# Kernel optimization log

Hardware: AMD Instinct MI355X
Metric: run time of the kernel (lower is better)

## Reference

```python
import jax, jax.numpy as jnp
import numpy as np

B, T, C = 2, 4096, 1024
H = 16            # n_head (== n_groups == n_kv_heads)
HD = C // H       # head_dim = 64
W = 256           # window_size
ROPE_BASE = 10000.0


def _rope(x):
    # x: (B, H, T, HD); rotate interleaved pairs with position along axis 2
    t = x.shape[2]
    inv_freq = 1.0 / (ROPE_BASE ** (jnp.arange(0, HD, 2, dtype=jnp.float32) / HD))  # (HD/2,)
    freqs = jnp.arange(t, dtype=jnp.float32)[:, None] * inv_freq[None, :]           # (T, HD/2)
    cos = jnp.cos(freqs)[None, None].astype(x.dtype)
    sin = jnp.sin(freqs)[None, None].astype(x.dtype)
    x1, x2 = x[..., 0::2], x[..., 1::2]
    o1 = x1 * cos - x2 * sin
    o2 = x1 * sin + x2 * cos
    return jnp.stack([o1, o2], axis=-1).reshape(x.shape)


def setup_inputs() -> dict:
    key = jax.random.key(0)
    ks = jax.random.split(key, 5)
    s = 1.0 / np.sqrt(C)
    return {
        "x": jax.random.normal(ks[0], (B, T, C), dtype=jnp.float32),
        "wq": jax.random.normal(ks[1], (C, C), dtype=jnp.float32) * s,
        "wk": jax.random.normal(ks[2], (C, C), dtype=jnp.float32) * s,
        "wv": jax.random.normal(ks[3], (C, C), dtype=jnp.float32) * s,
        "wo": jax.random.normal(ks[4], (C, C), dtype=jnp.float32) * s,
    }


def reference(x, wq, wk, wv, wo):
    # projections (Linear stores (out, in) -> x @ w.T)
    q = jnp.einsum('btc,oc->bto', x, wq).reshape(B, T, H, HD).transpose(0, 2, 1, 3)
    k = jnp.einsum('btc,oc->bto', x, wk).reshape(B, T, H, HD).transpose(0, 2, 1, 3)
    v = jnp.einsum('btc,oc->bto', x, wv).reshape(B, T, H, HD).transpose(0, 2, 1, 3)

    q = _rope(q)
    k = _rope(k)

    nW = T // W
    qw = q.reshape(B, H, nW, W, HD)
    kw = k.reshape(B, H, nW, W, HD)
    vw = v.reshape(B, H, nW, W, HD)

    scale = 1.0 / jnp.sqrt(jnp.asarray(HD, dtype=q.dtype))
    att = jnp.einsum('bhnqd,bhnkd->bhnqk', qw, kw) * scale   # per-window, no causal mask
    att = jax.nn.softmax(att, axis=-1)
    yw = jnp.einsum('bhnqk,bhnkd->bhnqd', att, vw)

    y = yw.reshape(B, H, T, HD).transpose(0, 2, 1, 3).reshape(B, T, C)
    return jnp.einsum('btc,oc->bto', y, wo)
```

## Files before the change

### kernel.cpp

```cpp
#include <hip/hip_runtime.h>
#include <math.h>

typedef float f32x4 __attribute__((ext_vector_type(4)));
typedef __bf16 bf16x8 __attribute__((ext_vector_type(8)));
typedef unsigned short ushort_t;

#define MFMA16(a, b, c) __builtin_amdgcn_mfma_f32_16x16x32_bf16((a), (b), (c), 0, 0, 0)

static __device__ __forceinline__ ushort_t f2bf(float f) {
  union { float f; unsigned u; } v; v.f = f;
  unsigned u = v.u;
  return (ushort_t)((u + 0x7FFFu + ((u >> 16) & 1u)) >> 16);
}
static __device__ __forceinline__ float bf2f(ushort_t h) {
  union { unsigned u; float f; } v; v.u = ((unsigned)h) << 16;
  return v.f;
}
static __device__ __forceinline__ void gl_lds16(const void* g, void* lds_uniform) {
  __builtin_amdgcn_global_load_lds(
      (const __attribute__((address_space(1))) unsigned int*)g,
      (__attribute__((address_space(3))) unsigned int*)lds_uniform, 16, 0, 0);
}

__global__ void prep(const float* __restrict__ x,
                     const float* __restrict__ wq, const float* __restrict__ wk,
                     const float* __restrict__ wv, const float* __restrict__ wo,
                     ushort_t* __restrict__ Xb, ushort_t* __restrict__ Wqb,
                     ushort_t* __restrict__ Wkb, ushort_t* __restrict__ Wvb,
                     ushort_t* __restrict__ Wob, float2* __restrict__ cs) {
  const int bid = blockIdx.x;
  if (bid < 12288) {
    const float* src;
    ushort_t* dst;
    int i;
    if (bid < 8192) {
      src = x; dst = Xb;
      i = bid * 256 + threadIdx.x;
    } else {
      const int wi = (bid - 8192) >> 10;
      src = (wi == 0) ? wq : (wi == 1) ? wk : (wi == 2) ? wv : wo;
      dst = (wi == 0) ? Wqb : (wi == 1) ? Wkb : (wi == 2) ? Wvb : Wob;
      i = ((bid - 8192) & 1023) * 256 + threadIdx.x;
    }
    f32x4 v = ((const f32x4*)src)[i];
    ushort4 o;
    o.x = f2bf(v.x); o.y = f2bf(v.y); o.z = f2bf(v.z); o.w = f2bf(v.w);
    ((ushort4*)dst)[i] = o;
  } else {
    int idx = (bid - 12288) * 256 + threadIdx.x;
    int pos = idx >> 5, i = idx & 31;
    double inv = exp2(-(double)i * 0.41524101186092029);
    double th = (double)pos * inv;
    double s, c;
    sincos(th, &s, &c);
    cs[idx] = make_float2((float)c, (float)s);
  }
}

template <int OUTBF>
__global__ __launch_bounds__(512, 2) void gemm8(
    const ushort_t* __restrict__ A,
    const ushort_t* __restrict__ W0, const ushort_t* __restrict__ W1, const ushort_t* __restrict__ W2,
    void* __restrict__ C0, void* __restrict__ C1, void* __restrict__ C2,
    int K, int N) {
  __shared__ __align__(16) char smem[98304];
  const int z = blockIdx.z;
  const ushort_t* W = (z == 0) ? W0 : (z == 1 ? W1 : W2);
  void* Cv = (z == 0) ? C0 : (z == 1 ? C1 : C2);

  const int t = threadIdx.x;
  const int lane = t & 63;
  const int l15 = lane & 15, quad = lane >> 4;
  const int wave = t >> 6;
  const int wm = wave >> 1, wn = wave & 1;
  const int bm = blockIdx.x, bn = blockIdx.y;

  const int r0 = t >> 3;
  const int gc = (t & 7) ^ (r0 & 7);
  const ushort_t* Ag = A + (size_t)(bm * 256 + r0) * K + gc * 8;
  const ushort_t* Wg = W + (size_t)(bn * 128 + r0) * K + gc * 8;
  const size_t p64K = (size_t)64 * K;
  char* ldsw = smem + wave * 1024;

  const int sl0 = (quad ^ (l15 & 7)) * 16;
  const int aoff = (wm * 64 + l15) * 128 + sl0;
  const int boff = 65536 + (wn * 64 + l15) * 128 + sl0;

  const int KT = K >> 6;

  const f32x4 zero4 = {0.f, 0.f, 0.f, 0.f};
  f32x4 acc[4][4];
#pragma unroll
  for (int i = 0; i < 4; ++i)
#pragma unroll
    for (int j = 0; j < 4; ++j) acc[i][j] = zero4;

  auto stA = [&](int buf, int p, int k0) {
    gl_lds16(Ag + p64K * p + k0, ldsw + buf * 32768 + p * 8192);
  };
  auto stB = [&](int buf, int p, int k0) {
    gl_lds16(Wg + p64K * p + k0, ldsw + 65536 + buf * 16384 + p * 8192);
  };

  stA(0, 0, 0); stA(0, 1, 0); stA(0, 2, 0); stA(0, 3, 0);
  stB(0, 0, 0); stB(0, 1, 0);
  stA(1, 0, 64); stA(1, 1, 64); stA(1, 2, 64); stA(1, 3, 64);
  asm volatile("s_waitcnt vmcnt(4)" ::: "memory");
  __builtin_amdgcn_s_barrier();

  bf16x8 af[4][2], bfr[4][2];

  for (int j = 0; j < KT; ++j) {
    const int cb = j & 1, nb = cb ^ 1;
    const char* Ab = smem + cb * 32768;
    const char* Bb = smem + cb * 16384;

#pragma unroll
    for (int m = 0; m < 4; ++m) {
      const int o = aoff + m * 2048;
      af[m][0] = *(const bf16x8*)(Ab + o);
      af[m][1] = *(const bf16x8*)(Ab + (o ^ 64));
    }
#pragma unroll
    for (int n = 0; n < 2; ++n) {
      const int o = boff + n * 2048;
      bfr[n][0] = *(const bf16x8*)(Bb + o);
      bfr[n][1] = *(const bf16x8*)(Bb + (o ^ 64));
    }
    if (j + 1 < KT) {
      stB(nb, 0, (j + 1) * 64);
      stB(nb, 1, (j + 1) * 64);
    }
    __builtin_amdgcn_s_barrier();
    asm volatile("s_waitcnt lgkmcnt(0)" ::: "memory");
    __builtin_amdgcn_sched_barrier(0);
    __builtin_amdgcn_s_setprio(1);
#pragma unroll
    for (int m = 0; m < 4; ++m)
#pragma unroll
      for (int n = 0; n < 2; ++n) {
        acc[m][n] = MFMA16(af[m][0], bfr[n][0], acc[m][n]);
        acc[m][n] = MFMA16(af[m][1], bfr[n][1], acc[m][n]);
      }
    __builtin_amdgcn_s_setprio(0);
    __builtin_amdgcn_sched_barrier(0);
    __builtin_amdgcn_s_barrier();

#pragma unroll
    for (int n = 2; n < 4; ++n) {
      const int o = boff + n * 2048;
      bfr[n][0] = *(const bf16x8*)(Bb + o);
      bfr[n][1] = *(const bf16x8*)(Bb + (o ^ 64));
    }
    if (j + 2 < KT) {
      stA(cb, 0, (j + 2) * 64);
      stA(cb, 1, (j + 2) * 64);
      stA(cb, 2, (j + 2) * 64);
      stA(cb, 3, (j + 2) * 64);
      asm volatile("s_waitcnt vmcnt(4)" ::: "memory");
    } else if (j + 1 < KT) {
      asm volatile("s_waitcnt vmcnt(0)" ::: "memory");
    }
    __builtin_amdgcn_s_barrier();
    asm volatile("s_waitcnt lgkmcnt(0)" ::: "memory");
    __builtin_amdgcn_sched_barrier(0);
    __builtin_amdgcn_s_setprio(1);
#pragma unroll
    for (int m = 0; m < 4; ++m)
#pragma unroll
      for (int n = 2; n < 4; ++n) {
        acc[m][n] = MFMA16(af[m][0], bfr[n][0], acc[m][n]);
        acc[m][n] = MFMA16(af[m][1], bfr[n][1], acc[m][n]);
      }
    __builtin_amdgcn_s_setprio(0);
    __builtin_amdgcn_sched_barrier(0);
    __builtin_amdgcn_s_barrier();
  }

  const int rbase = bm * 256 + wm * 64 + quad * 4;
  const int cbase = bn * 128 + wn * 64 + l15;
#pragma unroll
  for (int m = 0; m < 4; ++m)
#pragma unroll
    for (int n = 0; n < 4; ++n)
#pragma unroll
      for (int r = 0; r < 4; ++r) {
        size_t idx = (size_t)(rbase + m * 16 + r) * N + (cbase + n * 16);
        if (OUTBF)
          ((ushort_t*)Cv)[idx] = f2bf(acc[m][n][r]);
        else
          ((float*)Cv)[idx] = acc[m][n][r];
      }
}

static __device__ __forceinline__ void rope8(const ushort_t* __restrict__ g,
                                             ushort_t* __restrict__ lds,
                                             const float2* __restrict__ cs4, float scale) {
  uint4 raw = *(const uint4*)g;
  unsigned rw[4] = {raw.x, raw.y, raw.z, raw.w};
  ushort_t o[8];
#pragma unroll
  for (int m = 0; m < 4; ++m) {
    float x1 = bf2f((ushort_t)(rw[m] & 0xffffu));
    float x2 = bf2f((ushort_t)(rw[m] >> 16));
    float2 sc = cs4[m];
    o[2 * m]     = f2bf((x1 * sc.x - x2 * sc.y) * scale);
    o[2 * m + 1] = f2bf((x1 * sc.y + x2 * sc.x) * scale);
  }
  uint4 w;
  w.x = (unsigned)o[0] | ((unsigned)o[1] << 16);
  w.y = (unsigned)o[2] | ((unsigned)o[3] << 16);
  w.z = (unsigned)o[4] | ((unsigned)o[5] << 16);
  w.w = (unsigned)o[6] | ((unsigned)o[7] << 16);
  *(uint4*)lds = w;
}

__global__ __launch_bounds__(256, 2) void attn(
    const ushort_t* __restrict__ Qb, const ushort_t* __restrict__ Kb,
    const ushort_t* __restrict__ Vb, ushort_t* __restrict__ Yb,
    const float2* __restrict__ cs) {
  __shared__ __align__(16) ushort_t smem[27648];
  ushort_t* Qs = smem;
  ushort_t* Ks = smem + 9216;
  ushort_t* Vt = smem;
  ushort_t* Pc = smem + 16896;

  const int t = threadIdx.x;
  const int lane = t & 63, wave = t >> 6;
  const int l15 = lane & 15, quad = lane >> 4;
  const int win = blockIdx.x >> 1, slice = blockIdx.x & 1;
  const int h = blockIdx.y, b = blockIdx.z;
  const int kBase = win * 256, qBase = kBase + slice * 128;
  const size_t gbase = ((size_t)b * 4096) * 1024 + h * 64;

  const int sr = t >> 3;
  const int c0 = (t & 7) * 8;

#pragma unroll
  for (int p = 0; p < 4; ++p) {
    int r = p * 32 + sr;
    rope8(Qb + gbase + (size_t)(qBase + r) * 1024 + c0, Qs + r * 72 + c0,
          cs + (qBase + r) * 32 + (c0 >> 1), 0.125f);
  }
#pragma unroll
  for (int p = 0; p < 8; ++p) {
    int r = p * 32 + sr;
    rope8(Kb + gbase + (size_t)(kBase + r) * 1024 + c0, Ks + r * 72 + c0,
          cs + (kBase + r) * 32 + (c0 >> 1), 1.0f);
  }
  __syncthreads();

  const int qw = wave * 32;
  const f32x4 zero4 = {0.f, 0.f, 0.f, 0.f};
  f32x4 S[2][16];
#pragma unroll
  for (int i = 0; i < 2; ++i)
#pragma unroll
    for (int j = 0; j < 16; ++j) S[i][j] = zero4;
#pragma unroll
  for (int ks = 0; ks < 2; ++ks) {
    bf16x8 a0 = *(const bf16x8*)&Qs[(qw + l15) * 72 + ks * 32 + quad * 8];
    bf16x8 a1 = *(const bf16x8*)&Qs[(qw + 16 + l15) * 72 + ks * 32 + quad * 8];
#pragma unroll
    for (int j = 0; j < 16; ++j) {
      bf16x8 bk = *(const bf16x8*)&Ks[(j * 16 + l15) * 72 + ks * 32 + quad * 8];
      S[0][j] = MFMA16(a0, bk, S[0][j]);
      S[1][j] = MFMA16(a1, bk, S[1][j]);
    }
  }

  float linv[2][4];
#pragma unroll
  for (int i = 0; i < 2; ++i)
#pragma unroll
    for (int r = 0; r < 4; ++r) {
      float mx = S[i][0][r];
#pragma unroll
      for (int j = 1; j < 16; ++j) mx = fmaxf(mx, S[i][j][r]);
      mx = fmaxf(mx, __shfl_xor(mx, 1));
      mx = fmaxf(mx, __shfl_xor(mx, 2));
      mx = fmaxf(mx, __shfl_xor(mx, 4));
      mx = fmaxf(mx, __shfl_xor(mx, 8));
      float sum = 0.f;
#pragma unroll
      for (int j = 0; j < 16; ++j) {
        float e = __expf(S[i][j][r] - mx);
        S[i][j][r] = e;
        sum += e;
      }
      sum += __shfl_xor(sum, 1);
      sum += __shfl_xor(sum, 2);
      sum += __shfl_xor(sum, 4);
      sum += __shfl_xor(sum, 8);
      linv[i][r] = 1.0f / sum;
    }
  __syncthreads();

#pragma unroll
  for (int p = 0; p < 8; ++p) {
    int k = p * 32 + sr;
    uint4 raw = *(const uint4*)(Vb + gbase + (size_t)(kBase + k) * 1024 + c0);
    ushort_t vv[8];
    vv[0] = raw.x & 0xffffu; vv[1] = raw.x >> 16;
    vv[2] = raw.y & 0xffffu; vv[3] = raw.y >> 16;
    vv[4] = raw.z & 0xffffu; vv[5] = raw.z >> 16;
    vv[6] = raw.w & 0xffffu; vv[7] = raw.w >> 16;
#pragma unroll
    for (int e = 0; e < 8; ++e) {
      int ee = (e + (t & 7)) & 7;
      Vt[(c0 + ee) * 264 + k] = vv[ee];
    }
  }

  auto writeP = [&](int kc) {
#pragma unroll
    for (int i = 0; i < 2; ++i)
#pragma unroll
      for (int jj = 0; jj < 4; ++jj) {
        int j = kc * 4 + jj;
#pragma unroll
        for (int r = 0; r < 4; ++r)
          Pc[(qw + i * 16 + quad * 4 + r) * 72 + jj * 16 + l15] = f2bf(S[i][j][r]);
      }
  };

  writeP(0);
  __syncthreads();

  f32x4 O[2][4];
#pragma unroll
  for (int i = 0; i < 2; ++i)
#pragma unroll
    for (int jd = 0; jd < 4; ++jd) O[i][jd] = zero4;

  for (int kc = 0; kc < 4; ++kc) {
#pragma unroll
    for (int ks = 0; ks < 2; ++ks) {
      bf16x8 a0 = *(const bf16x8*)&Pc[(qw + l15) * 72 + ks * 32 + quad * 8];
      bf16x8 a1 = *(const bf16x8*)&Pc[(qw + 16 + l15) * 72 + ks * 32 + quad * 8];
#pragma unroll
      for (int jd = 0; jd < 4; ++jd) {
        bf16x8 bv = *(const bf16x8*)&Vt[(jd * 16 + l15) * 264 + kc * 64 + ks * 32 + quad * 8];
        O[0][jd] = MFMA16(a0, bv, O[0][jd]);
        O[1][jd] = MFMA16(a1, bv, O[1][jd]);
      }
    }
    if (kc < 3) {
      __syncthreads();
      writeP(kc + 1);
      __syncthreads();
    }
  }

#pragma unroll
  for (int i = 0; i < 2; ++i)
#pragma unroll
    for (int jd = 0; jd < 4; ++jd)
#pragma unroll
      for (int r = 0; r < 4; ++r) {
        int row = qBase + qw + i * 16 + quad * 4 + r;
        int col = jd * 16 + l15;
        Yb[gbase + (size_t)row * 1024 + col] = f2bf(O[i][jd][r] * linv[i][r]);
      }
}

extern "C" void kernel_launch(void* const* d_in, const int* in_sizes, int n_in,
                              void* d_out, int out_size, void* d_ws, size_t ws_size,
                              hipStream_t stream) {
  (void)in_sizes; (void)n_in; (void)out_size; (void)ws_size;
  const float* x  = (const float*)d_in[0];
  const float* wq = (const float*)d_in[1];
  const float* wk = (const float*)d_in[2];
  const float* wv = (const float*)d_in[3];
  const float* wo = (const float*)d_in[4];

  char* ws = (char*)d_ws;
  ushort_t* Xb  = (ushort_t*)(ws);
  ushort_t* Wqb = (ushort_t*)(ws + 16777216);
  ushort_t* Wkb = Wqb + 1048576;
  ushort_t* Wvb = Wkb + 1048576;
  ushort_t* Wob = Wvb + 1048576;
  ushort_t* Qb  = (ushort_t*)(ws + 25165824);
  ushort_t* Kb  = Qb + 8388608;
  ushort_t* Vb  = Kb + 8388608;
  ushort_t* Yb  = Vb + 8388608;
  float2*   cs  = (float2*)(ws + 92274688);

  prep<<<dim3(12800), dim3(256), 0, stream>>>(x, wq, wk, wv, wo,
                                              Xb, Wqb, Wkb, Wvb, Wob, cs);

  gemm8<1><<<dim3(32, 8, 3), dim3(512), 0, stream>>>(
      Xb, Wqb, Wkb, Wvb, (void*)Qb, (void*)Kb, (void*)Vb, 1024, 1024);

  attn<<<dim3(32, 16, 2), dim3(256), 0, stream>>>(Qb, Kb, Vb, Yb, cs);

  gemm8<0><<<dim3(32, 8, 1), dim3(512), 0, stream>>>(
      Yb, Wob, Wob, Wob, d_out, d_out, d_out, 1024, 1024);
}
```

Before: 208.0 us.

## Enlarge GEMM block tile to 256x256 with four-phase pipelined K loop

The GEMM block tile grows from 256x128 to 256x256. Each wave now computes 128x64 outputs with an 8x4 accumulator array, and the grid halves along N. The K loop is split into four MFMA phases that interleave LDS fragment reads with staggered global-to-LDS prefetches of A and B, using a double-buffered 128KB shared memory. This raises arithmetic intensity and cuts global/LDS traffic per FLOP, at the cost of more registers, more LDS (likely one block per CU), and fewer blocks (384 and 128 instead of 768 and 256).

```diff
diff --git a/kernel.cpp b/kernel.cpp
--- a/kernel.cpp
+++ b/kernel.cpp
@@ -63,7 +63,7 @@
     const ushort_t* __restrict__ W0, const ushort_t* __restrict__ W1, const ushort_t* __restrict__ W2,
     void* __restrict__ C0, void* __restrict__ C1, void* __restrict__ C2,
     int K, int N) {
-  __shared__ __align__(16) char smem[98304];
+  __shared__ __align__(16) char smem[131072];
   const int z = blockIdx.z;
   const ushort_t* W = (z == 0) ? W0 : (z == 1 ? W1 : W2);
   void* Cv = (z == 0) ? C0 : (z == 1 ? C1 : C2);
@@ -72,64 +72,66 @@
   const int lane = t & 63;
   const int l15 = lane & 15, quad = lane >> 4;
   const int wave = t >> 6;
-  const int wm = wave >> 1, wn = wave & 1;
+  const int wm = wave >> 2, wn = wave & 3;
   const int bm = blockIdx.x, bn = blockIdx.y;
 
   const int r0 = t >> 3;
   const int gc = (t & 7) ^ (r0 & 7);
-  const ushort_t* Ag = A + (size_t)(bm * 256 + r0) * K + gc * 8;
-  const ushort_t* Wg = W + (size_t)(bn * 128 + r0) * K + gc * 8;
-  const size_t p64K = (size_t)64 * K;
+  const ushort_t* AgB = A + (size_t)(bm * 256 + r0) * K + gc * 8;
+  const ushort_t* WgB = W + (size_t)(bn * 256 + r0) * K + gc * 8;
+  const size_t q64K = (size_t)64 * K;
   char* ldsw = smem + wave * 1024;
 
   const int sl0 = (quad ^ (l15 & 7)) * 16;
-  const int aoff = (wm * 64 + l15) * 128 + sl0;
-  const int boff = 65536 + (wn * 64 + l15) * 128 + sl0;
+  const int aoff = (wm * 128 + l15) * 128 + sl0;
+  const int boff = 32768 + (wn * 64 + l15) * 128 + sl0;
 
   const int KT = K >> 6;
 
   const f32x4 zero4 = {0.f, 0.f, 0.f, 0.f};
-  f32x4 acc[4][4];
-#pragma unroll
-  for (int i = 0; i < 4; ++i)
+  f32x4 acc[8][4];
+#pragma unroll
+  for (int i = 0; i < 8; ++i)
 #pragma unroll
     for (int j = 0; j < 4; ++j) acc[i][j] = zero4;
 
-  auto stA = [&](int buf, int p, int k0) {
-    gl_lds16(Ag + p64K * p + k0, ldsw + buf * 32768 + p * 8192);
+  auto stA = [&](int buf, int q, int kt) {
+    gl_lds16(AgB + (size_t)q * q64K + (size_t)kt * 64, ldsw + buf * 65536 + q * 8192);
   };
-  auto stB = [&](int buf, int p, int k0) {
-    gl_lds16(Wg + p64K * p + k0, ldsw + 65536 + buf * 16384 + p * 8192);
+  auto stB = [&](int buf, int q, int kt) {
+    gl_lds16(WgB + (size_t)q * q64K + (size_t)kt * 64, ldsw + buf * 65536 + 32768 + q * 8192);
   };
 
-  stA(0, 0, 0); stA(0, 1, 0); stA(0, 2, 0); stA(0, 3, 0);
-  stB(0, 0, 0); stB(0, 1, 0);
-  stA(1, 0, 64); stA(1, 1, 64); stA(1, 2, 64); stA(1, 3, 64);
-  asm volatile("s_waitcnt vmcnt(4)" ::: "memory");
+#pragma unroll
+  for (int q = 0; q < 4; ++q) stA(0, q, 0);
+#pragma unroll
+  for (int q = 0; q < 4; ++q) stB(0, q, 0);
+#pragma unroll
+  for (int q = 0; q < 4; ++q) stA(1, q, 1);
+#pragma unroll
+  for (int q = 0; q < 4; ++q) stB(1, q, 1);
+  asm volatile("s_waitcnt vmcnt(8)" ::: "memory");
   __builtin_amdgcn_s_barrier();
 
-  bf16x8 af[4][2], bfr[4][2];
+  bf16x8 af[4][2], b01[2][2], b23[2][2];
 
   for (int j = 0; j < KT; ++j) {
-    const int cb = j & 1, nb = cb ^ 1;
-    const char* Ab = smem + cb * 32768;
-    const char* Bb = smem + cb * 16384;
+    const int cb = j & 1;
+    const char* bufb = smem + cb * 65536;
+    const bool pf = (j + 2 < KT);
+    const int k2 = j + 2;
 
 #pragma unroll
     for (int m = 0; m < 4; ++m) {
       const int o = aoff + m * 2048;
-      af[m][0] = *(const bf16x8*)(Ab + o);
-      af[m][1] = *(const bf16x8*)(Ab + (o ^ 64));
+      af[m][0] = *(const bf16x8*)(bufb + o);
+      af[m][1] = *(const bf16x8*)(bufb + (o ^ 64));
     }
 #pragma unroll
     for (int n = 0; n < 2; ++n) {
       const int o = boff + n * 2048;
-      bfr[n][0] = *(const bf16x8*)(Bb + o);
-      bfr[n][1] = *(const bf16x8*)(Bb + (o ^ 64));
-    }
-    if (j + 1 < KT) {
-      stB(nb, 0, (j + 1) * 64);
-      stB(nb, 1, (j + 1) * 64);
+      b01[n][0] = *(const bf16x8*)(bufb + o);
+      b01[n][1] = *(const bf16x8*)(bufb + (o ^ 64));
     }
     __builtin_amdgcn_s_barrier();
     asm volatile("s_waitcnt lgkmcnt(0)" ::: "memory");
@@ -139,48 +141,82 @@
     for (int m = 0; m < 4; ++m)
 #pragma unroll
       for (int n = 0; n < 2; ++n) {
-        acc[m][n] = MFMA16(af[m][0], bfr[n][0], acc[m][n]);
-        acc[m][n] = MFMA16(af[m][1], bfr[n][1], acc[m][n]);
+        acc[m][n] = MFMA16(af[m][0], b01[n][0], acc[m][n]);
+        acc[m][n] = MFMA16(af[m][1], b01[n][1], acc[m][n]);
       }
     __builtin_amdgcn_s_setprio(0);
     __builtin_amdgcn_sched_barrier(0);
     __builtin_amdgcn_s_barrier();
 
 #pragma unroll
-    for (int n = 2; n < 4; ++n) {
-      const int o = boff + n * 2048;
-      bfr[n][0] = *(const bf16x8*)(Bb + o);
-      bfr[n][1] = *(const bf16x8*)(Bb + (o ^ 64));
-    }
-    if (j + 2 < KT) {
-      stA(cb, 0, (j + 2) * 64);
-      stA(cb, 1, (j + 2) * 64);
-      stA(cb, 2, (j + 2) * 64);
-      stA(cb, 3, (j + 2) * 64);
-      asm volatile("s_waitcnt vmcnt(4)" ::: "memory");
+    for (int n = 0; n < 2; ++n) {
+      const int o = boff + (n + 2) * 2048;
+      b23[n][0] = *(const bf16x8*)(bufb + o);
+      b23[n][1] = *(const bf16x8*)(bufb + (o ^ 64));
+    }
+    if (pf) { stA(cb, 0, k2); stA(cb, 2, k2); }
+    __builtin_amdgcn_s_barrier();
+    asm volatile("s_waitcnt lgkmcnt(0)" ::: "memory");
+    __builtin_amdgcn_sched_barrier(0);
+    __builtin_amdgcn_s_setprio(1);
+#pragma unroll
+    for (int m = 0; m < 4; ++m)
+#pragma unroll
+      for (int n = 0; n < 2; ++n) {
+        acc[m][n + 2] = MFMA16(af[m][0], b23[n][0], acc[m][n + 2]);
+        acc[m][n + 2] = MFMA16(af[m][1], b23[n][1], acc[m][n + 2]);
+      }
+    __builtin_amdgcn_s_setprio(0);
+    __builtin_amdgcn_sched_barrier(0);
+    __builtin_amdgcn_s_barrier();
+
+#pragma unroll
+    for (int m = 0; m < 4; ++m) {
+      const int o = aoff + (m + 4) * 2048;
+      af[m][0] = *(const bf16x8*)(bufb + o);
+      af[m][1] = *(const bf16x8*)(bufb + (o ^ 64));
+    }
+    if (pf) { stB(cb, 0, k2); stB(cb, 1, k2); }
+    __builtin_amdgcn_s_barrier();
+    asm volatile("s_waitcnt lgkmcnt(0)" ::: "memory");
+    __builtin_amdgcn_sched_barrier(0);
+    __builtin_amdgcn_s_setprio(1);
+#pragma unroll
+    for (int m = 0; m < 4; ++m)
+#pragma unroll
+      for (int n = 0; n < 2; ++n) {
+        acc[m + 4][n] = MFMA16(af[m][0], b01[n][0], acc[m + 4][n]);
+        acc[m + 4][n] = MFMA16(af[m][1], b01[n][1], acc[m + 4][n]);
+      }
+    __builtin_amdgcn_s_setprio(0);
+    __builtin_amdgcn_sched_barrier(0);
+    __builtin_amdgcn_s_barrier();
+
+    if (pf) {
+      stA(cb, 1, k2); stA(cb, 3, k2);
+      stB(cb, 2, k2); stB(cb, 3, k2);
+      asm volatile("s_waitcnt vmcnt(8)" ::: "memory");
     } else if (j + 1 < KT) {
       asm volatile("s_waitcnt vmcnt(0)" ::: "memory");
     }
     __builtin_amdgcn_s_barrier();
-    asm volatile("s_waitcnt lgkmcnt(0)" ::: "memory");
-    __builtin_amdgcn_sched_barrier(0);
     __builtin_amdgcn_s_setprio(1);
 #pragma unroll
     for (int m = 0; m < 4; ++m)
 #pragma unroll
-      for (int n = 2; n < 4; ++n) {
-        acc[m][n] = MFMA16(af[m][0], bfr[n][0], acc[m][n]);
-        acc[m][n] = MFMA16(af[m][1], bfr[n][1], acc[m][n]);
+      for (int n = 0; n < 2; ++n) {
+        acc[m + 4][n + 2] = MFMA16(af[m][0], b23[n][0], acc[m + 4][n + 2]);
+        acc[m + 4][n + 2] = MFMA16(af[m][1], b23[n][1], acc[m + 4][n + 2]);
       }
     __builtin_amdgcn_s_setprio(0);
     __builtin_amdgcn_sched_barrier(0);
     __builtin_amdgcn_s_barrier();
   }
 
-  const int rbase = bm * 256 + wm * 64 + quad * 4;
-  const int cbase = bn * 128 + wn * 64 + l15;
-#pragma unroll
-  for (int m = 0; m < 4; ++m)
+  const int rbase = bm * 256 + wm * 128 + quad * 4;
+  const int cbase = bn * 256 + wn * 64 + l15;
+#pragma unroll
+  for (int m = 0; m < 8; ++m)
 #pragma unroll
     for (int n = 0; n < 4; ++n)
 #pragma unroll
@@ -389,11 +425,11 @@
   prep<<<dim3(12800), dim3(256), 0, stream>>>(x, wq, wk, wv, wo,
                                               Xb, Wqb, Wkb, Wvb, Wob, cs);
 
-  gemm8<1><<<dim3(32, 8, 3), dim3(512), 0, stream>>>(
+  gemm8<1><<<dim3(32, 4, 3), dim3(512), 0, stream>>>(
       Xb, Wqb, Wkb, Wvb, (void*)Qb, (void*)Kb, (void*)Vb, 1024, 1024);
 
   attn<<<dim3(32, 16, 2), dim3(256), 0, stream>>>(Qb, Kb, Vb, Yb, cs);
 
-  gemm8<0><<<dim3(32, 8, 1), dim3(512), 0, stream>>>(
+  gemm8<0><<<dim3(32, 4, 1), dim3(512), 0, stream>>>(
       Yb, Wob, Wob, Wob, d_out, d_out, d_out, 1024, 1024);
 }
```

New measurement: 226.8 us. 1.09x slower.
